# Kernel tuning notes

Measured on AMD Instinct MI355X. Metric: run time of the kernel, lower is better.

## Reference

```python
import jax, jax.numpy as jnp
import numpy as np

TAU = 0.5
EPS = 1e-8


def setup_inputs() -> dict:
    key = jax.random.key(0)
    k1, k2 = jax.random.split(key)
    N, D = 16384, 128
    Tx1 = jax.random.normal(k1, (N, D), dtype=jnp.float32)
    Tx2 = jax.random.normal(k2, (N, D), dtype=jnp.float32)
    return {"Tx1": Tx1, "Tx2": Tx2}


def reference(Tx1, Tx2):
    n = Tx1.shape[0]
    # squared pairwise distances ||Tx1_i - Tx2_j||^2 via the expansion trick
    # (matches torch.cdist(...).pow(2), clamped to be non-negative)
    sq1 = jnp.sum(Tx1 * Tx1, axis=1)  # [n]
    sq2 = jnp.sum(Tx2 * Tx2, axis=1)  # [n]
    cross = jnp.einsum('id,jd->ij', Tx1, Tx2)  # [n, n]
    sq_dists = jnp.maximum(sq1[:, None] + sq2[None, :] - 2.0 * cross, 0.0)
    repulsion = jnp.mean(jnp.exp(-sq_dists / (2.0 * TAU)), axis=1)  # [n]
    pos_sq = jnp.sum((Tx1 - Tx2) ** 2, axis=1)  # [n]
    attraction = jnp.exp(-pos_sq / (2.0 * TAU))  # [n]
    loss = jnp.mean(jnp.log1p(repulsion / (attraction + EPS)))
    return loss, jnp.mean(attraction), jnp.mean(repulsion)
```

## Files before the change

kernel.cpp:

```cpp
#include <hip/hip_runtime.h>
#include <hip/hip_bf16.h>


#define EPS 1e-8f
#define D_DIM 128
#define INV_LN2 1.44269504088896f
#define QSCALE 16.0f
#define KQ 0.011271992507f
#define NCHUNK 8
#define TCOLS 64
#define NT 32
#define NPH 16
#define BM 128

typedef __attribute__((ext_vector_type(4))) int   i32x4;
typedef __attribute__((ext_vector_type(4))) float f32x4;

typedef __attribute__((address_space(1))) const unsigned int gu32_t;
typedef __attribute__((address_space(3))) unsigned int lu32_t;

static __device__ inline void gload_lds16(const void* g, void* l) {
    __builtin_amdgcn_global_load_lds((gu32_t*)g, (lu32_t*)l, 16, 0, 0);
}

static __device__ inline int q8(float x) {
    float r = rintf(x * QSCALE);
    r = fminf(fmaxf(r, -127.f), 127.f);
    return (int)r;
}

static __device__ inline int imax2(int a, int b) { return a > b ? a : b; }

__global__ __launch_bounds__(256) void prep_kernel(
    const float* __restrict__ X1, const float* __restrict__ X2,
    unsigned char* __restrict__ Q1, unsigned char* __restrict__ Q2,
    float* __restrict__ sq1n, float* __restrict__ sq2,
    float* __restrict__ att)
{
    const int w = threadIdx.x >> 6;
    const int l = threadIdx.x & 63;
    const int i = blockIdx.x * 4 + w;
    const float2 a = ((const float2*)(X1 + (size_t)i * D_DIM))[l];
    const float2 b = ((const float2*)(X2 + (size_t)i * D_DIM))[l];

    const int qa0 = q8(a.x), qa1 = q8(a.y);
    const int qb0 = q8(b.x), qb1 = q8(b.y);
    ((ushort*)(Q1 + (size_t)i * D_DIM))[l] =
        (ushort)((qa0 & 0xff) | ((qa1 & 0xff) << 8));
    ((ushort*)(Q2 + (size_t)i * D_DIM))[l] =
        (ushort)((qb0 & 0xff) | ((qb1 & 0xff) << 8));

    float s1 = a.x * a.x + a.y * a.y;
    float s2 = b.x * b.x + b.y * b.y;
    float dx = a.x - b.x, dy = a.y - b.y;
    float ps = dx * dx + dy * dy;
    #pragma unroll
    for (int m = 32; m; m >>= 1) {
        s1 += __shfl_xor(s1, m, 64);
        s2 += __shfl_xor(s2, m, 64);
        ps += __shfl_xor(ps, m, 64);
    }
    if (l == 0) {
        sq1n[i] = -s1 * INV_LN2;
        sq2[i]  =  s2 * INV_LN2;
        att[i]  = __expf(-ps);
    }
}

__global__ __launch_bounds__(512, 4) void cross_kernel(
    const unsigned char* __restrict__ Q1, const unsigned char* __restrict__ Q2,
    const float* __restrict__ sq1n, const float* __restrict__ sq2,
    float* __restrict__ partials, int Ntot)
{
    __shared__ char  bufs[4][8192];
    __shared__ float ldsS1[BM];
    __shared__ float ldsS2[NT * TCOLS];

    const int t    = threadIdx.x;
    const int lane = t & 63;
    const int wid  = t >> 6;
    const int wy   = wid >> 2;
    const int wx   = wid & 3;
    const int lr   = lane & 15;
    const int kg   = lane >> 4;

    const int brow = blockIdx.y * BM;
    const int ccol = blockIdx.x * (NT * TCOLS);

    const char* gA = (const char*)(Q1 + (size_t)brow * D_DIM);
    const char* gB = (const char*)(Q2 + (size_t)ccol * D_DIM);

    #pragma unroll
    for (int it = 0; it < 2; ++it) {
        const unsigned L   = it * 8192u + wid * 1024u + lane * 16u;
        const unsigned src = L ^ (((L >> 7) & 7u) << 4);
        gload_lds16(gA + src, bufs[it] + wid * 1024);
    }
    if (t < BM) ldsS1[t] = sq1n[brow + t];
    ((float4*)ldsS2)[t] = ((const float4*)(sq2 + ccol))[t];
    __syncthreads();

    i32x4 aR[8];
    #pragma unroll
    for (int m = 0; m < 4; ++m) {
        const int lrow = m * 16 + lr;
        #pragma unroll
        for (int kc = 0; kc < 2; ++kc) {
            const unsigned addr = (unsigned)(lrow * 128 + kc * 64 + kg * 16)
                                  ^ (((unsigned)(lrow & 7)) << 4);
            aR[m * 2 + kc] = *(const i32x4*)(bufs[wy] + addr);
        }
    }
    float4 ns1[4];
    #pragma unroll
    for (int m = 0; m < 4; ++m)
        ns1[m] = *(const float4*)(ldsS1 + wy * 64 + m * 16 + kg * 4);
    float thr = -1e30f;
    #pragma unroll
    for (int m = 0; m < 4; ++m)
        thr = fmaxf(thr, fmaxf(fmaxf(ns1[m].x, ns1[m].y),
                               fmaxf(ns1[m].z, ns1[m].w)));
    __syncthreads();

    #pragma unroll
    for (int tile = 0; tile < 4; ++tile) {
        const char* gBt = gB + (size_t)tile * (TCOLS * 128u);
        const unsigned L   = wid * 1024u + lane * 16u;
        const unsigned src = L ^ (((L >> 7) & 7u) << 4);
        gload_lds16(gBt + src, bufs[tile] + wid * 1024);
    }
    asm volatile("s_waitcnt vmcnt(2)" ::: "memory");
    __builtin_amdgcn_s_barrier();
    __builtin_amdgcn_sched_barrier(0);

    const int  brW   = wx * 16 + lr;
    const unsigned bAddr0 = (unsigned)(brW * 128 + 0 * 64 + kg * 16)
                            ^ (((unsigned)(brW & 7)) << 4);
    const unsigned bAddr1 = (unsigned)(brW * 128 + 1 * 64 + kg * 16)
                            ^ (((unsigned)(brW & 7)) << 4);

    float p[4][4];
    #pragma unroll
    for (int m = 0; m < 4; ++m)
        #pragma unroll
        for (int r = 0; r < 4; ++r)
            p[m][r] = 0.f;

#define EPILOG(ACC, S2)                                                      \
    {                                                                        \
        int ia = imax2(imax2(ACC[0][0], ACC[0][1]), imax2(ACC[0][2], ACC[0][3])); \
        int ib = imax2(imax2(ACC[1][0], ACC[1][1]), imax2(ACC[1][2], ACC[1][3])); \
        int ic = imax2(imax2(ACC[2][0], ACC[2][1]), imax2(ACC[2][2], ACC[2][3])); \
        int id = imax2(imax2(ACC[3][0], ACC[3][1]), imax2(ACC[3][2], ACC[3][3])); \
        const int imx = imax2(imax2(ia, ib), imax2(ic, id));                 \
        if (__any(fmaf((float)imx, KQ, thr) - (S2) > -149.0f)) {             \
            _Pragma("unroll")                                                \
            for (int m = 0; m < 4; ++m)                                      \
                _Pragma("unroll")                                            \
                for (int r = 0; r < 4; ++r)                                  \
                    p[m][r] += __builtin_amdgcn_exp2f(                       \
                        fmaf((float)ACC[m][r], KQ,                           \
                             ((const float*)&ns1[m])[r]) - (S2));            \
        }                                                                    \
    }

    for (int k = 0; k < NPH; ++k) {
        char* slotE = bufs[(k & 1) * 2 + 0];
        char* slotO = bufs[(k & 1) * 2 + 1];

        i32x4 bE0 = *(const i32x4*)(slotE + bAddr0);
        i32x4 bE1 = *(const i32x4*)(slotE + bAddr1);
        i32x4 bO0 = *(const i32x4*)(slotO + bAddr0);
        i32x4 bO1 = *(const i32x4*)(slotO + bAddr1);
        const float s2E = ldsS2[(2 * k)     * TCOLS + wx * 16 + lr];
        const float s2O = ldsS2[(2 * k + 1) * TCOLS + wx * 16 + lr];

        asm volatile("s_waitcnt lgkmcnt(0)" ::: "memory");
        __builtin_amdgcn_sched_barrier(0);
        __builtin_amdgcn_s_barrier();
        __builtin_amdgcn_sched_barrier(0);

        if (k + 1 < NPH) {
            #pragma unroll
            for (int half = 0; half < 2; ++half) {
                const int tile = 2 * (k + 2) + half;
                if (tile < NT) {
                    const char* gBn = gB + (size_t)tile * (TCOLS * 128u);
                    const unsigned L   = wid * 1024u + lane * 16u;
                    const unsigned src = L ^ (((L >> 7) & 7u) << 4);
                    gload_lds16(gBn + src,
                                ((half == 0) ? slotE : slotO) + wid * 1024);
                }
            }
        }

        i32x4 accE[4], accO[4];
        #pragma unroll
        for (int m = 0; m < 4; ++m) { accE[m] = (i32x4){0,0,0,0};
                                      accO[m] = (i32x4){0,0,0,0}; }
        __builtin_amdgcn_s_setprio(1);
        #pragma unroll
        for (int m = 0; m < 4; ++m)
            accE[m] = __builtin_amdgcn_mfma_i32_16x16x64_i8(
                aR[m * 2 + 0], bE0, accE[m], 0, 0, 0);
        #pragma unroll
        for (int m = 0; m < 4; ++m)
            accE[m] = __builtin_amdgcn_mfma_i32_16x16x64_i8(
                aR[m * 2 + 1], bE1, accE[m], 0, 0, 0);
        #pragma unroll
        for (int m = 0; m < 4; ++m)
            accO[m] = __builtin_amdgcn_mfma_i32_16x16x64_i8(
                aR[m * 2 + 0], bO0, accO[m], 0, 0, 0);
        #pragma unroll
        for (int m = 0; m < 4; ++m)
            accO[m] = __builtin_amdgcn_mfma_i32_16x16x64_i8(
                aR[m * 2 + 1], bO1, accO[m], 0, 0, 0);
        __builtin_amdgcn_s_setprio(0);

        EPILOG(accE, s2E);
        EPILOG(accO, s2O);

        if (k + 1 < NPH) {
            if (k + 2 < NPH) {
                asm volatile("s_waitcnt vmcnt(2)" ::: "memory");
            } else {
                asm volatile("s_waitcnt vmcnt(0)" ::: "memory");
            }
            __builtin_amdgcn_s_barrier();
            __builtin_amdgcn_sched_barrier(0);
        }
    }
#undef EPILOG

    const size_t plane = (size_t)(blockIdx.x * 4 + wx) * (size_t)Ntot;
    #pragma unroll
    for (int m = 0; m < 4; ++m) {
        #pragma unroll
        for (int r = 0; r < 4; ++r) {
            float v = p[m][r];
            v += __shfl_xor(v, 1, 64);
            v += __shfl_xor(v, 2, 64);
            v += __shfl_xor(v, 4, 64);
            v += __shfl_xor(v, 8, 64);
            if (lr == 0)
                partials[plane + brow + wy * 64 + m * 16 + kg * 4 + r] = v;
        }
    }
}

__global__ __launch_bounds__(256) void rowsum_kernel(
    const float* __restrict__ partials, const float* __restrict__ att,
    float* __restrict__ blocksums, int N)
{
    __shared__ float sm[3][4];
    const int i = blockIdx.x * 256 + threadIdx.x;
    const float inv = 1.0f / (float)N;
    float s = 0.f;
    #pragma unroll
    for (int pl = 0; pl < 4 * NCHUNK; ++pl)
        s += partials[(size_t)pl * N + i];
    const float rp = s * inv;
    const float at = att[i];
    float ls = log1pf(rp / (at + EPS));
    float sa = at;
    float sr = rp;
    #pragma unroll
    for (int m = 32; m; m >>= 1) {
        ls += __shfl_xor(ls, m, 64);
        sa += __shfl_xor(sa, m, 64);
        sr += __shfl_xor(sr, m, 64);
    }
    const int w = threadIdx.x >> 6, lane = threadIdx.x & 63;
    if (lane == 0) { sm[0][w] = ls; sm[1][w] = sa; sm[2][w] = sr; }
    __syncthreads();
    if (threadIdx.x < 3) {
        const float v = sm[threadIdx.x][0] + sm[threadIdx.x][1]
                      + sm[threadIdx.x][2] + sm[threadIdx.x][3];
        blocksums[threadIdx.x * 64 + blockIdx.x] = v;
    }
}

__global__ __launch_bounds__(192) void final_kernel(
    const float* __restrict__ blocksums, float* __restrict__ out, int N)
{
    const int w = threadIdx.x >> 6;
    const int lane = threadIdx.x & 63;
    float v = blocksums[w * 64 + lane];
    #pragma unroll
    for (int m = 32; m; m >>= 1) v += __shfl_xor(v, m, 64);
    if (lane == 0) out[w] = v / (float)N;
}

extern "C" void kernel_launch(void* const* d_in, const int* in_sizes, int n_in,
                              void* d_out, int out_size, void* d_ws, size_t ws_size,
                              hipStream_t stream)
{
    const float* X1 = (const float*)d_in[0];
    const float* X2 = (const float*)d_in[1];
    const int N = in_sizes[0] / D_DIM;
    float* out = (float*)d_out;

    char* ws = (char*)d_ws;
    unsigned char* Q1 = (unsigned char*)ws;
    unsigned char* Q2 = Q1 + (size_t)N * D_DIM;
    float* sq1n = (float*)(ws + (size_t)2 * N * D_DIM);
    float* sq2 = sq1n + N;
    float* att = sq2 + N;
    float* partials = att + N;
    float* blocksums = partials + (size_t)4 * NCHUNK * N;

    prep_kernel<<<N / 4, 256, 0, stream>>>(X1, X2, Q1, Q2, sq1n, sq2, att);
    dim3 grid(NCHUNK, N / BM);
    cross_kernel<<<grid, 512, 0, stream>>>(Q1, Q2, sq1n, sq2, partials, N);
    rowsum_kernel<<<N / 256, 256, 0, stream>>>(partials, att, blocksums, N);
    final_kernel<<<1, 192, 0, stream>>>(blocksums, out, N);
}
```

Baseline: 50.43 us.

## Fold final reduction into rowsum via last-block atomic counter; drop S1 LDS staging

Removes the separate final_kernel launch by having the last rowsum block, chosen through an atomic counter that prep_kernel resets, do the final cross-block reduction. The cross kernel also loads its row norms straight from global memory instead of staging them through LDS, and adds a sched_barrier after the sync. The aim is to cut one kernel launch and a little LDS traffic, in exchange for an atomic, memory fences and volatile reads.

```diff
diff --git a/kernel.cpp b/kernel.cpp
--- a/kernel.cpp
+++ b/kernel.cpp
@@ -35,8 +35,9 @@
     const float* __restrict__ X1, const float* __restrict__ X2,
     unsigned char* __restrict__ Q1, unsigned char* __restrict__ Q2,
     float* __restrict__ sq1n, float* __restrict__ sq2,
-    float* __restrict__ att)
+    float* __restrict__ att, int* __restrict__ counter)
 {
+    if (blockIdx.x == 0 && threadIdx.x == 0) *counter = 0;
     const int w = threadIdx.x >> 6;
     const int l = threadIdx.x & 63;
     const int i = blockIdx.x * 4 + w;
@@ -73,7 +74,6 @@
     float* __restrict__ partials, int Ntot)
 {
     __shared__ char  bufs[4][8192];
-    __shared__ float ldsS1[BM];
     __shared__ float ldsS2[NT * TCOLS];
 
     const int t    = threadIdx.x;
@@ -96,7 +96,6 @@
         const unsigned src = L ^ (((L >> 7) & 7u) << 4);
         gload_lds16(gA + src, bufs[it] + wid * 1024);
     }
-    if (t < BM) ldsS1[t] = sq1n[brow + t];
     ((float4*)ldsS2)[t] = ((const float4*)(sq2 + ccol))[t];
     __syncthreads();
 
@@ -114,13 +113,14 @@
     float4 ns1[4];
     #pragma unroll
     for (int m = 0; m < 4; ++m)
-        ns1[m] = *(const float4*)(ldsS1 + wy * 64 + m * 16 + kg * 4);
+        ns1[m] = *(const float4*)(sq1n + brow + wy * 64 + m * 16 + kg * 4);
     float thr = -1e30f;
     #pragma unroll
     for (int m = 0; m < 4; ++m)
         thr = fmaxf(thr, fmaxf(fmaxf(ns1[m].x, ns1[m].y),
                                fmaxf(ns1[m].z, ns1[m].w)));
     __syncthreads();
+    __builtin_amdgcn_sched_barrier(0);
 
     #pragma unroll
     for (int tile = 0; tile < 4; ++tile) {
@@ -250,9 +250,11 @@
 
 __global__ __launch_bounds__(256) void rowsum_kernel(
     const float* __restrict__ partials, const float* __restrict__ att,
-    float* __restrict__ blocksums, int N)
+    float* __restrict__ blocksums, int* __restrict__ counter,
+    float* __restrict__ out, int N)
 {
     __shared__ float sm[3][4];
+    __shared__ int isLast;
     const int i = blockIdx.x * 256 + threadIdx.x;
     const float inv = 1.0f / (float)N;
     float s = 0.f;
@@ -278,17 +280,21 @@
                       + sm[threadIdx.x][2] + sm[threadIdx.x][3];
         blocksums[threadIdx.x * 64 + blockIdx.x] = v;
     }
-}
-
-__global__ __launch_bounds__(192) void final_kernel(
-    const float* __restrict__ blocksums, float* __restrict__ out, int N)
-{
-    const int w = threadIdx.x >> 6;
-    const int lane = threadIdx.x & 63;
-    float v = blocksums[w * 64 + lane];
-    #pragma unroll
-    for (int m = 32; m; m >>= 1) v += __shfl_xor(v, m, 64);
-    if (lane == 0) out[w] = v / (float)N;
+    __syncthreads();
+    if (threadIdx.x == 0) {
+        __threadfence();
+        isLast = (atomicAdd(counter, 1) == (int)gridDim.x - 1);
+    }
+    __syncthreads();
+    if (isLast && threadIdx.x < 192) {
+        __threadfence();
+        const int ww = threadIdx.x >> 6;
+        const int ll = threadIdx.x & 63;
+        float v = ((volatile const float*)blocksums)[ww * 64 + ll];
+        #pragma unroll
+        for (int m = 32; m; m >>= 1) v += __shfl_xor(v, m, 64);
+        if (ll == 0) out[ww] = v / (float)N;
+    }
 }
 
 extern "C" void kernel_launch(void* const* d_in, const int* in_sizes, int n_in,
@@ -308,10 +314,12 @@
     float* att = sq2 + N;
     float* partials = att + N;
     float* blocksums = partials + (size_t)4 * NCHUNK * N;
-
-    prep_kernel<<<N / 4, 256, 0, stream>>>(X1, X2, Q1, Q2, sq1n, sq2, att);
+    int*   counter   = (int*)(blocksums + 192);
+
+    prep_kernel<<<N / 4, 256, 0, stream>>>(X1, X2, Q1, Q2, sq1n, sq2, att,
+                                           counter);
     dim3 grid(NCHUNK, N / BM);
     cross_kernel<<<grid, 512, 0, stream>>>(Q1, Q2, sq1n, sq2, partials, N);
-    rowsum_kernel<<<N / 256, 256, 0, stream>>>(partials, att, blocksums, N);
-    final_kernel<<<1, 192, 0, stream>>>(blocksums, out, N);
-}
+    rowsum_kernel<<<N / 256, 256, 0, stream>>>(partials, att, blocksums,
+                                               counter, out, N);
+}
```

Measured after the change: 51.37 us. Within noise of the previous version (+1.9%).
